# Optimization experiments

Hardware: AMD Instinct MI355X
Metric: run time of the kernel (lower is better)

The kernel has to match this reference:

```python
import jax, jax.numpy as jnp
import numpy as np

N_NODES = 100000
N_EDGES = 1600000
IN_FEATS = 128
N_HIDDEN = 128
N_CLASSES = 16


def setup_inputs() -> dict:
    key = jax.random.key(0)
    ks = jax.random.split(key, 10)
    features = jax.random.normal(ks[0], (N_NODES, IN_FEATS), dtype=jnp.float32)
    src = jax.random.randint(ks[1], (N_EDGES,), 0, N_NODES, dtype=jnp.int32)
    dst = jax.random.randint(ks[2], (N_EDGES,), 0, N_NODES, dtype=jnp.int32)
    # Glorot-ish init for the three GraphConv layers
    def glorot(k, fan_in, fan_out):
        s = (2.0 / (fan_in + fan_out)) ** 0.5
        return jax.random.normal(k, (fan_in, fan_out), dtype=jnp.float32) * s
    W0 = glorot(ks[3], IN_FEATS, N_HIDDEN)
    b0 = jnp.zeros((N_HIDDEN,), jnp.float32)
    W1 = glorot(ks[4], N_HIDDEN, N_HIDDEN)
    b1 = jnp.zeros((N_HIDDEN,), jnp.float32)
    W2 = glorot(ks[5], N_HIDDEN, N_CLASSES)
    b2 = jnp.zeros((N_CLASSES,), jnp.float32)
    return {"features": features, "src": src, "dst": dst,
            "W0": W0, "b0": b0, "W1": W1, "b1": b1, "W2": W2, "b2": b2}


def _graph_conv(h, src, dst, src_norm, dst_norm, W, b, act):
    # DGL GraphConv, norm='both':
    # out = D_dst^{-1/2} * sum_{(u->v) in E} (D_src^{-1/2} h)_u W  + b
    h = h * src_norm[:, None]           # [N, F] scale by out-degree^-1/2
    hw = h @ W                          # [N, F_out] transform before gather (F_out <= F here)
    agg = jax.ops.segment_sum(hw[src], dst, num_segments=h.shape[0])  # scatter-add over edges
    out = agg * dst_norm[:, None] + b
    return act(out)


def reference(features, src, dst, W0, b0, W1, b1, W2, b2):
    N = features.shape[0]
    ones = jnp.ones(src.shape[0], dtype=jnp.float32)
    out_deg = jnp.clip(jax.ops.segment_sum(ones, src, num_segments=N), 1.0)
    in_deg = jnp.clip(jax.ops.segment_sum(ones, dst, num_segments=N), 1.0)
    src_norm = out_deg ** -0.5
    dst_norm = in_deg ** -0.5

    relu = jax.nn.relu
    pos_sigmoid = lambda x: jax.nn.sigmoid(x) + 1e-8

    h = features.astype(jnp.float32)
    h = _graph_conv(h, src, dst, src_norm, dst_norm, W0, b0, relu)
    h = _graph_conv(h, src, dst, src_norm, dst_norm, W1, b1, relu)
    h = _graph_conv(h, src, dst, src_norm, dst_norm, W2, b2, pos_sigmoid)
    return h
```

## Files before the change

### kernel.cpp

```cpp
#include <hip/hip_runtime.h>
#include <hip/hip_bf16.h>


constexpr int BLK = 256;
constexpr int CH = 8192;

typedef __attribute__((ext_vector_type(8))) short s8v;
typedef __attribute__((ext_vector_type(4))) float f4v;

__device__ __forceinline__ float bflo(unsigned int u) { return __uint_as_float(u << 16); }
__device__ __forceinline__ float bfhi(unsigned int u) { return __uint_as_float(u & 0xffff0000u); }
__device__ __forceinline__ unsigned int bfr(float f) {
    unsigned int u = __float_as_uint(f);
    return (u + 0x7fffu + ((u >> 16) & 1u)) >> 16;
}
__device__ __forceinline__ unsigned int bfpack(float lo, float hi) {
    unsigned int ul = __float_as_uint(lo), uh = __float_as_uint(hi);
    unsigned int rl = (ul + 0x7fffu + ((ul >> 16) & 1u)) >> 16;
    unsigned int rh = (uh + 0x7fffu + ((uh >> 16) & 1u)) & 0xffff0000u;
    return rl | rh;
}

__global__ __launch_bounds__(256) void k_pcount(const int* __restrict__ src, const int* __restrict__ dst,
                                                int* __restrict__ pmat_d, int* __restrict__ pmat_s,
                                                int E, int NB) {
    __shared__ int hd[1024], hs[1024];
    for (int i = threadIdx.x; i < 1024; i += 256) { hd[i] = 0; hs[i] = 0; }
    __syncthreads();
    int b = blockIdx.x;
    int e0 = b * CH, e1 = min(e0 + CH, E);
    for (int e = e0 + threadIdx.x; e < e1; e += 256) {
        atomicAdd(&hd[dst[e] >> 7], 1);
        atomicAdd(&hs[src[e] >> 7], 1);
    }
    __syncthreads();
    for (int i = threadIdx.x; i < NB; i += 256) {
        pmat_d[(size_t)b * NB + i] = hd[i];
        pmat_s[(size_t)b * NB + i] = hs[i];
    }
}

__global__ __launch_bounds__(1024) void k_pscan1(const int* __restrict__ pmat_d, const int* __restrict__ pmat_s,
                                                 int* __restrict__ bbase_d, int* __restrict__ bbase_s,
                                                 int NB, int nblk) {
    const int* pmat = blockIdx.x ? pmat_s : pmat_d;
    int* bbase = blockIdx.x ? bbase_s : bbase_d;
    __shared__ int s[1024];
    int t = threadIdx.x;
    int tot = 0;
    if (t < NB) {
#pragma unroll 8
        for (int b = 0; b < nblk; b++) tot += pmat[(size_t)b * NB + t];
    }
    s[t] = (t < NB) ? tot : 0;
    __syncthreads();
    for (int d = 1; d < 1024; d <<= 1) {
        int x = (t >= d) ? s[t - d] : 0;
        __syncthreads();
        s[t] += x;
        __syncthreads();
    }
    if (t < NB) {
        bbase[t] = s[t] - tot;
        if (t == NB - 1) bbase[NB] = s[t];
    }
}

__global__ __launch_bounds__(256) void k_pscan2(const int* __restrict__ pmat_d, const int* __restrict__ pmat_s,
                                                const int* __restrict__ bbase_d, const int* __restrict__ bbase_s,
                                                int* __restrict__ omat_d, int* __restrict__ omat_s,
                                                int NB, int nblk) {
    int which = blockIdx.x & 1;
    int t = (blockIdx.x >> 1) * 256 + threadIdx.x;
    const int* pmat = which ? pmat_s : pmat_d;
    const int* bbase = which ? bbase_s : bbase_d;
    int* omat = which ? omat_s : omat_d;
    if (t >= NB) return;
    int run = bbase[t];
#pragma unroll 8
    for (int b = 0; b < nblk; b++) {
        size_t idx = (size_t)b * NB + t;
        omat[idx] = run;
        run += pmat[idx];
    }
}

__global__ __launch_bounds__(256) void k_pscatter(const int* __restrict__ src, const int* __restrict__ dst,
                                                  const int* __restrict__ omat_d, const int* __restrict__ omat_s,
                                                  unsigned int* __restrict__ ebuf_d, unsigned char* __restrict__ ebuf_s,
                                                  int E, int NB) {
    __shared__ int cd[1024], cs[1024];
    int b = blockIdx.x;
    for (int i = threadIdx.x; i < NB; i += 256) {
        cd[i] = omat_d[(size_t)b * NB + i];
        cs[i] = omat_s[(size_t)b * NB + i];
    }
    __syncthreads();
    int e0 = b * CH, e1 = min(e0 + CH, E);
    for (int e = e0 + threadIdx.x; e < e1; e += 256) {
        int s_ = src[e], d_ = dst[e];
        int pd = atomicAdd(&cd[d_ >> 7], 1);
        ebuf_d[pd] = (unsigned)s_ | ((unsigned)(d_ & 127) << 17);
        int ps = atomicAdd(&cs[s_ >> 7], 1);
        ebuf_s[ps] = (unsigned char)(s_ & 127);
    }
}

__global__ __launch_bounds__(256) void k_bcount(const unsigned char* __restrict__ ebuf_s,
                                                const int* __restrict__ bbase_s,
                                                float* __restrict__ srcn, int N) {
    __shared__ int cnt[128];
    int k = blockIdx.x;
    if (threadIdx.x < 128) cnt[threadIdx.x] = 0;
    __syncthreads();
    int beg = bbase_s[k], end = bbase_s[k + 1];
    for (int i = beg + threadIdx.x; i < end; i += 256) atomicAdd(&cnt[ebuf_s[i]], 1);
    __syncthreads();
    if (threadIdx.x < 128) {
        int v = k * 128 + threadIdx.x;
        if (v < N) {
            int c = cnt[threadIdx.x];
            if (c < 1) c = 1;
            srcn[v] = rsqrtf((float)c);
        }
    }
}

__global__ __launch_bounds__(256) void k_sortcsr(const unsigned int* __restrict__ ebuf,
                                                 const int* __restrict__ bbase,
                                                 int* __restrict__ csr, int* __restrict__ rowptr,
                                                 int N, int E) {
    __shared__ unsigned int rec[4096];
    __shared__ unsigned int sorted[4096];
    __shared__ int cnt[128];
    __shared__ int wstart[129];
    __shared__ int wcur[128];
    int k = blockIdx.x, tx = threadIdx.x;
    int ebeg = bbase[k];
    int ecnt = bbase[k + 1] - ebeg;
    if (ecnt > 4096) ecnt = 4096;
    if (tx < 128) cnt[tx] = 0;
    __syncthreads();
    for (int i = tx; i < ecnt; i += 256) {
        unsigned int r = ebuf[ebeg + i];
        rec[i] = r;
        atomicAdd(&cnt[(r >> 17) & 127], 1);
    }
    __syncthreads();
    if (tx < 128) wcur[tx] = cnt[tx];
    __syncthreads();
    for (int d = 1; d < 128; d <<= 1) {
        int x = (tx < 128 && tx >= d) ? wcur[tx - d] : 0;
        __syncthreads();
        if (tx < 128) wcur[tx] += x;
        __syncthreads();
    }
    if (tx < 128) wstart[tx] = wcur[tx] - cnt[tx];
    if (tx == 127) wstart[128] = wcur[127];
    __syncthreads();
    if (tx < 128) wcur[tx] = wstart[tx];
    __syncthreads();
    for (int i = tx; i < ecnt; i += 256) {
        unsigned int r = rec[i];
        int p = atomicAdd(&wcur[(r >> 17) & 127], 1);
        sorted[p] = r & 0x1FFFFu;
    }
    __syncthreads();
    for (int i = tx; i < ecnt; i += 256) csr[ebeg + i] = (int)sorted[i];
    if (tx < 128) {
        int v = k * 128 + tx;
        if (v < N) rowptr[v] = ebeg + wstart[tx];
    }
    if (k == (int)gridDim.x - 1 && tx == 0) rowptr[N] = E;
}

__global__ void k_wt3(const float* __restrict__ W0, const float* __restrict__ W1, const float* __restrict__ W2,
                      unsigned short* __restrict__ Wt0, unsigned short* __restrict__ Wt1,
                      unsigned short* __restrict__ Wt2) {
    int b = blockIdx.x;
    const float* W; unsigned short* Wt; int total, base;
    if (b < 64)      { W = W0; Wt = Wt0; total = 16384; base = b * 256; }
    else if (b < 128){ W = W1; Wt = Wt1; total = 16384; base = (b - 64) * 256; }
    else             { W = W2; Wt = Wt2; total = 2048;  base = (b - 128) * 256; }
    int i = base + threadIdx.x;
    if (i < total) {
        int Ncol = total >> 7;
        int c = i >> 7, k = i & 127;
        Wt[i] = (unsigned short)bfr(W[k * Ncol + c]);
    }
}

template <int NT, int F32IN>
__global__ __launch_bounds__(256) void k_gemm_mfma(const unsigned short* __restrict__ Ab,
                                                   const float* __restrict__ Af,
                                                   const float* __restrict__ srcn,
                                                   const unsigned short* __restrict__ Wt,
                                                   unsigned short* __restrict__ outb, int M) {
    __shared__ unsigned short As[64 * 128];
    __shared__ unsigned short Ws[NT * 16 * 128];
    int tx = threadIdx.x;
    int row0 = blockIdx.x * 64;
    for (int p = 0; p < NT; ++p) {
        int r = p * 16 + (tx >> 4);
        int c = tx & 15;
        int cs = c ^ (r & 7);
        *(uint4*)(&Ws[(r * 16 + cs) * 8]) = *(const uint4*)(Wt + (size_t)r * 128 + c * 8);
    }
    for (int p = 0; p < 4; ++p) {
        int r = p * 16 + (tx >> 4);
        int c = tx & 15;
        int cs = c ^ (r & 7);
        int gr = row0 + r;
        uint4 v = make_uint4(0u, 0u, 0u, 0u);
        if (gr < M) {
            if (F32IN) {
                const float4* pf = (const float4*)(Af + (size_t)gr * 128 + c * 8);
                float4 a = pf[0], b = pf[1];
                float s = srcn[gr];
                v.x = bfpack(a.x * s, a.y * s);
                v.y = bfpack(a.z * s, a.w * s);
                v.z = bfpack(b.x * s, b.y * s);
                v.w = bfpack(b.z * s, b.w * s);
            } else {
                v = *(const uint4*)(Ab + (size_t)gr * 128 + c * 8);
            }
        }
        *(uint4*)(&As[(r * 16 + cs) * 8]) = v;
    }
    __syncthreads();

    int w = tx >> 6, l = tx & 63;
    int lr = l & 15, lg = l >> 4;
    f4v acc[NT];
#pragma unroll
    for (int nt = 0; nt < NT; ++nt) { acc[nt][0] = 0.f; acc[nt][1] = 0.f; acc[nt][2] = 0.f; acc[nt][3] = 0.f; }

    int ar = w * 16 + lr;
#pragma unroll
    for (int kk = 0; kk < 4; ++kk) {
        s8v af = *(const s8v*)(&As[(ar * 16 + ((kk * 4 + lg) ^ (ar & 7))) * 8]);
#pragma unroll
        for (int nt = 0; nt < NT; ++nt) {
            int br = nt * 16 + lr;
            s8v bf = *(const s8v*)(&Ws[(br * 16 + ((kk * 4 + lg) ^ (br & 7))) * 8]);
            acc[nt] = __builtin_amdgcn_mfma_f32_16x16x32_bf16(af, bf, acc[nt], 0, 0, 0);
        }
    }
#pragma unroll
    for (int nt = 0; nt < NT; ++nt) {
#pragma unroll
        for (int i = 0; i < 4; ++i) {
            int R = row0 + w * 16 + lg * 4 + i;
            if (R < M) {
                int col = nt * 16 + lr;
                outb[(size_t)R * (NT * 16) + col] = (unsigned short)bfr(acc[nt][i]);
            }
        }
    }
}

__global__ __launch_bounds__(256) void k_aggN(const unsigned short* __restrict__ hw,
                                              const int* __restrict__ csr,
                                              const int* __restrict__ rowptr,
                                              const float* __restrict__ srcn,
                                              const float* __restrict__ bias,
                                              unsigned short* __restrict__ out, int N) {
    int t = blockIdx.x * 256 + threadIdx.x;
    int v = t >> 4, sub = t & 15;
    if (v >= N) return;
    int s0 = rowptr[v], s1 = rowptr[v + 1];

    float a0 = 0.f, a1 = 0.f, a2 = 0.f, a3 = 0.f, a4 = 0.f, a5 = 0.f, a6 = 0.f, a7 = 0.f;
#define ACC8(V)                                                         \
    a0 += bflo(V.x); a1 += bfhi(V.x); a2 += bflo(V.y); a3 += bfhi(V.y); \
    a4 += bflo(V.z); a5 += bfhi(V.z); a6 += bflo(V.w); a7 += bfhi(V.w);
    int e = s0;
    for (; e + 4 <= s1; e += 4) {
        int x0 = csr[e], x1 = csr[e + 1], x2 = csr[e + 2], x3 = csr[e + 3];
        uint4 v0 = *(const uint4*)(hw + (size_t)x0 * 128 + sub * 8);
        uint4 v1 = *(const uint4*)(hw + (size_t)x1 * 128 + sub * 8);
        uint4 v2 = *(const uint4*)(hw + (size_t)x2 * 128 + sub * 8);
        uint4 v3 = *(const uint4*)(hw + (size_t)x3 * 128 + sub * 8);
        ACC8(v0) ACC8(v1) ACC8(v2) ACC8(v3)
    }
    for (; e < s1; ++e) {
        int x0 = csr[e];
        uint4 v0 = *(const uint4*)(hw + (size_t)x0 * 128 + sub * 8);
        ACC8(v0)
    }
#undef ACC8
    int deg = s1 - s0;
    if (deg < 1) deg = 1;
    float dn = rsqrtf((float)deg);
    float4 b0 = *(const float4*)(bias + sub * 8);
    float4 b1 = *(const float4*)(bias + sub * 8 + 4);
    float sn = srcn[v];
    float o0 = fmaxf(a0 * dn + b0.x, 0.f) * sn, o1 = fmaxf(a1 * dn + b0.y, 0.f) * sn;
    float o2 = fmaxf(a2 * dn + b0.z, 0.f) * sn, o3 = fmaxf(a3 * dn + b0.w, 0.f) * sn;
    float o4 = fmaxf(a4 * dn + b1.x, 0.f) * sn, o5 = fmaxf(a5 * dn + b1.y, 0.f) * sn;
    float o6 = fmaxf(a6 * dn + b1.z, 0.f) * sn, o7 = fmaxf(a7 * dn + b1.w, 0.f) * sn;
    uint4 o;
    o.x = bfpack(o0, o1); o.y = bfpack(o2, o3);
    o.z = bfpack(o4, o5); o.w = bfpack(o6, o7);
    *(uint4*)(out + (size_t)v * 128 + sub * 8) = o;
}

__global__ __launch_bounds__(256) void k_agg16(const unsigned short* __restrict__ hw,
                                               const int* __restrict__ csr,
                                               const int* __restrict__ rowptr,
                                               const float* __restrict__ bias,
                                               float* __restrict__ out, int N) {
    int t = blockIdx.x * 256 + threadIdx.x;
    int v = t >> 2, q = t & 3;
    if (v >= N) return;
    int s0 = rowptr[v], s1 = rowptr[v + 1];
    float a0 = 0.f, a1 = 0.f, a2 = 0.f, a3 = 0.f;
#define ACC4(V)                                                         \
    a0 += bflo(V.x); a1 += bfhi(V.x); a2 += bflo(V.y); a3 += bfhi(V.y);
    int e = s0;
    for (; e + 4 <= s1; e += 4) {
        int x0 = csr[e], x1 = csr[e + 1], x2 = csr[e + 2], x3 = csr[e + 3];
        uint2 v0 = *(const uint2*)(hw + (size_t)x0 * 16 + q * 4);
        uint2 v1 = *(const uint2*)(hw + (size_t)x1 * 16 + q * 4);
        uint2 v2 = *(const uint2*)(hw + (size_t)x2 * 16 + q * 4);
        uint2 v3 = *(const uint2*)(hw + (size_t)x3 * 16 + q * 4);
        ACC4(v0) ACC4(v1) ACC4(v2) ACC4(v3)
    }
    for (; e < s1; ++e) {
        int x0 = csr[e];
        uint2 v0 = *(const uint2*)(hw + (size_t)x0 * 16 + q * 4);
        ACC4(v0)
    }
#undef ACC4
    int deg = s1 - s0;
    if (deg < 1) deg = 1;
    float dn = rsqrtf((float)deg);
    float4 b = *(const float4*)(bias + q * 4);
    float o0 = 1.f / (1.f + __expf(-(a0 * dn + b.x))) + 1e-8f;
    float o1 = 1.f / (1.f + __expf(-(a1 * dn + b.y))) + 1e-8f;
    float o2 = 1.f / (1.f + __expf(-(a2 * dn + b.z))) + 1e-8f;
    float o3 = 1.f / (1.f + __expf(-(a3 * dn + b.w))) + 1e-8f;
    *(float4*)(out + (size_t)v * 16 + q * 4) = make_float4(o0, o1, o2, o3);
}

extern "C" void kernel_launch(void* const* d_in, const int* in_sizes, int n_in,
                              void* d_out, int out_size, void* d_ws, size_t ws_size,
                              hipStream_t stream) {
    const float* features = (const float*)d_in[0];
    const int*   src      = (const int*)d_in[1];
    const int*   dst      = (const int*)d_in[2];
    const float* W0       = (const float*)d_in[3];
    const float* b0       = (const float*)d_in[4];
    const float* W1       = (const float*)d_in[5];
    const float* b1       = (const float*)d_in[6];
    const float* W2       = (const float*)d_in[7];
    const float* b2       = (const float*)d_in[8];
    float* out = (float*)d_out;

    const int N = in_sizes[0] / 128;
    const int E = in_sizes[1];
    const int NB = (N + 127) >> 7;
    const int nblk = (E + CH - 1) / CH;

    char* ws = (char*)d_ws;
    size_t off = 0;
    auto alloc = [&](size_t bytes) -> char* {
        char* p = ws + off;
        off += (bytes + 255) / 256 * 256;
        return p;
    };
    int* pmat_d  = (int*)alloc((size_t)nblk * NB * 4);
    int* pmat_s  = (int*)alloc((size_t)nblk * NB * 4);
    int* omat_d  = (int*)alloc((size_t)nblk * NB * 4);
    int* omat_s  = (int*)alloc((size_t)nblk * NB * 4);
    int* bbase_d = (int*)alloc((size_t)(NB + 1) * 4);
    int* bbase_s = (int*)alloc((size_t)(NB + 1) * 4);
    unsigned int*  ebuf_d = (unsigned int*)alloc((size_t)E * 4);
    unsigned char* ebuf_s = (unsigned char*)alloc((size_t)E);
    int* csr     = (int*)alloc((size_t)E * 4);
    int* rowptr  = (int*)alloc((size_t)(N + 1) * 4);
    float* srcn  = (float*)alloc((size_t)N * 4);
    unsigned short* Wt0 = (unsigned short*)alloc(128 * 128 * 2);
    unsigned short* Wt1 = (unsigned short*)alloc(128 * 128 * 2);
    unsigned short* Wt2 = (unsigned short*)alloc(16 * 128 * 2);
    unsigned short* B1 = (unsigned short*)alloc((size_t)N * 128 * 2);
    unsigned short* B2 = (unsigned short*)alloc((size_t)N * 128 * 2);
    unsigned short* HW16 = (unsigned short*)alloc((size_t)N * 16 * 2);
    (void)ws_size; (void)n_in; (void)out_size;

    k_pcount<<<nblk, 256, 0, stream>>>(src, dst, pmat_d, pmat_s, E, NB);
    k_pscan1<<<2, 1024, 0, stream>>>(pmat_d, pmat_s, bbase_d, bbase_s, NB, nblk);
    k_pscan2<<<2 * ((NB + 255) / 256), 256, 0, stream>>>(pmat_d, pmat_s, bbase_d, bbase_s, omat_d, omat_s, NB, nblk);
    k_pscatter<<<nblk, 256, 0, stream>>>(src, dst, omat_d, omat_s, ebuf_d, ebuf_s, E, NB);
    k_bcount<<<NB, 256, 0, stream>>>(ebuf_s, bbase_s, srcn, N);
    k_sortcsr<<<NB, 256, 0, stream>>>(ebuf_d, bbase_d, csr, rowptr, N, E);
    k_wt3<<<136, 256, 0, stream>>>(W0, W1, W2, Wt0, Wt1, Wt2);

    int gb = (N + 63) / 64;
    int anb = (N * 16 + 255) / 256;
    int a16b = (N * 4 + 255) / 256;

    k_gemm_mfma<8, 1><<<gb, 256, 0, stream>>>(nullptr, features, srcn, Wt0, B2, N);
    k_aggN<<<anb, 256, 0, stream>>>(B2, csr, rowptr, srcn, b0, B1, N);
    k_gemm_mfma<8, 0><<<gb, 256, 0, stream>>>(B1, nullptr, nullptr, Wt1, B2, N);
    k_aggN<<<anb, 256, 0, stream>>>(B2, csr, rowptr, srcn, b1, B1, N);
    k_gemm_mfma<1, 0><<<gb, 256, 0, stream>>>(B1, nullptr, nullptr, Wt2, HW16, N);
    k_agg16<<<a16b, 256, 0, stream>>>(HW16, csr, rowptr, b2, out, N);
}
```

Baseline: 351.7 us.

## Fuse preprocessing kernels, pad CSR rows to 4, and loop GEMM over strips

Merges the two scan kernels into one and fuses CSR sort, source-degree counting and weight transpose into a single multi-role launch, which removes several launches. CSR rows are padded to a multiple of four with a dummy zeroed node row at index N. The aggregation kernels can then load four neighbour indices as one int4 and drop the scalar tail loop. The GEMM kernel now processes four 64-row strips per block, so the weight tile staged in shared memory is reused across strips. The costs are extra padded gathers of the zero row and a cap of 3584 edges per 128-node bucket, which could truncate rows on skewed graphs.

```diff
diff --git a/kernel.cpp b/kernel.cpp
--- a/kernel.cpp
+++ b/kernel.cpp
@@ -40,11 +40,14 @@
     }
 }
 
-__global__ __launch_bounds__(1024) void k_pscan1(const int* __restrict__ pmat_d, const int* __restrict__ pmat_s,
-                                                 int* __restrict__ bbase_d, int* __restrict__ bbase_s,
-                                                 int NB, int nblk) {
+__global__ __launch_bounds__(1024) void k_pscan(const int* __restrict__ pmat_d, const int* __restrict__ pmat_s,
+                                                int* __restrict__ bbase_d, int* __restrict__ bbase_s,
+                                                int* __restrict__ omat_d, int* __restrict__ omat_s,
+                                                unsigned short* __restrict__ B2pad, unsigned short* __restrict__ HW16pad,
+                                                int N, int NB, int nblk) {
     const int* pmat = blockIdx.x ? pmat_s : pmat_d;
     int* bbase = blockIdx.x ? bbase_s : bbase_d;
+    int* omat  = blockIdx.x ? omat_s : omat_d;
     __shared__ int s[1024];
     int t = threadIdx.x;
     int tot = 0;
@@ -61,27 +64,20 @@
         __syncthreads();
     }
     if (t < NB) {
-        bbase[t] = s[t] - tot;
+        int base = s[t] - tot;
+        bbase[t] = base;
         if (t == NB - 1) bbase[NB] = s[t];
-    }
-}
-
-__global__ __launch_bounds__(256) void k_pscan2(const int* __restrict__ pmat_d, const int* __restrict__ pmat_s,
-                                                const int* __restrict__ bbase_d, const int* __restrict__ bbase_s,
-                                                int* __restrict__ omat_d, int* __restrict__ omat_s,
-                                                int NB, int nblk) {
-    int which = blockIdx.x & 1;
-    int t = (blockIdx.x >> 1) * 256 + threadIdx.x;
-    const int* pmat = which ? pmat_s : pmat_d;
-    const int* bbase = which ? bbase_s : bbase_d;
-    int* omat = which ? omat_s : omat_d;
-    if (t >= NB) return;
-    int run = bbase[t];
+        int run = base;
 #pragma unroll 8
-    for (int b = 0; b < nblk; b++) {
-        size_t idx = (size_t)b * NB + t;
-        omat[idx] = run;
-        run += pmat[idx];
+        for (int b = 0; b < nblk; b++) {
+            size_t idx = (size_t)b * NB + t;
+            omat[idx] = run;
+            run += pmat[idx];
+        }
+    }
+    if (blockIdx.x == 1) {
+        if (t < 128) B2pad[(size_t)N * 128 + t] = 0;
+        if (t < 16)  HW16pad[(size_t)N * 16 + t] = 0;
     }
 }
 
@@ -106,87 +102,92 @@
     }
 }
 
-__global__ __launch_bounds__(256) void k_bcount(const unsigned char* __restrict__ ebuf_s,
-                                                const int* __restrict__ bbase_s,
-                                                float* __restrict__ srcn, int N) {
-    __shared__ int cnt[128];
-    int k = blockIdx.x;
-    if (threadIdx.x < 128) cnt[threadIdx.x] = 0;
-    __syncthreads();
-    int beg = bbase_s[k], end = bbase_s[k + 1];
-    for (int i = beg + threadIdx.x; i < end; i += 256) atomicAdd(&cnt[ebuf_s[i]], 1);
-    __syncthreads();
-    if (threadIdx.x < 128) {
-        int v = k * 128 + threadIdx.x;
-        if (v < N) {
-            int c = cnt[threadIdx.x];
-            if (c < 1) c = 1;
-            srcn[v] = rsqrtf((float)c);
-        }
-    }
-}
-
-__global__ __launch_bounds__(256) void k_sortcsr(const unsigned int* __restrict__ ebuf,
-                                                 const int* __restrict__ bbase,
-                                                 int* __restrict__ csr, int* __restrict__ rowptr,
-                                                 int N, int E) {
-    __shared__ unsigned int rec[4096];
-    __shared__ unsigned int sorted[4096];
-    __shared__ int cnt[128];
-    __shared__ int wstart[129];
-    __shared__ int wcur[128];
-    int k = blockIdx.x, tx = threadIdx.x;
-    int ebeg = bbase[k];
-    int ecnt = bbase[k + 1] - ebeg;
-    if (ecnt > 4096) ecnt = 4096;
-    if (tx < 128) cnt[tx] = 0;
-    __syncthreads();
-    for (int i = tx; i < ecnt; i += 256) {
-        unsigned int r = ebuf[ebeg + i];
-        rec[i] = r;
-        atomicAdd(&cnt[(r >> 17) & 127], 1);
-    }
-    __syncthreads();
-    if (tx < 128) wcur[tx] = cnt[tx];
-    __syncthreads();
-    for (int d = 1; d < 128; d <<= 1) {
-        int x = (tx < 128 && tx >= d) ? wcur[tx - d] : 0;
-        __syncthreads();
-        if (tx < 128) wcur[tx] += x;
-        __syncthreads();
-    }
-    if (tx < 128) wstart[tx] = wcur[tx] - cnt[tx];
-    if (tx == 127) wstart[128] = wcur[127];
-    __syncthreads();
-    if (tx < 128) wcur[tx] = wstart[tx];
-    __syncthreads();
-    for (int i = tx; i < ecnt; i += 256) {
-        unsigned int r = rec[i];
-        int p = atomicAdd(&wcur[(r >> 17) & 127], 1);
-        sorted[p] = r & 0x1FFFFu;
-    }
-    __syncthreads();
-    for (int i = tx; i < ecnt; i += 256) csr[ebeg + i] = (int)sorted[i];
-    if (tx < 128) {
-        int v = k * 128 + tx;
-        if (v < N) rowptr[v] = ebeg + wstart[tx];
-    }
-    if (k == (int)gridDim.x - 1 && tx == 0) rowptr[N] = E;
-}
-
-__global__ void k_wt3(const float* __restrict__ W0, const float* __restrict__ W1, const float* __restrict__ W2,
-                      unsigned short* __restrict__ Wt0, unsigned short* __restrict__ Wt1,
-                      unsigned short* __restrict__ Wt2) {
-    int b = blockIdx.x;
-    const float* W; unsigned short* Wt; int total, base;
-    if (b < 64)      { W = W0; Wt = Wt0; total = 16384; base = b * 256; }
-    else if (b < 128){ W = W1; Wt = Wt1; total = 16384; base = (b - 64) * 256; }
-    else             { W = W2; Wt = Wt2; total = 2048;  base = (b - 128) * 256; }
-    int i = base + threadIdx.x;
-    if (i < total) {
-        int Ncol = total >> 7;
-        int c = i >> 7, k = i & 127;
-        Wt[i] = (unsigned short)bfr(W[k * Ncol + c]);
+__global__ __launch_bounds__(256) void k_build(const unsigned int* __restrict__ ebuf_d,
+                                               const int* __restrict__ bbase_d,
+                                               const unsigned char* __restrict__ ebuf_s,
+                                               const int* __restrict__ bbase_s,
+                                               int* __restrict__ csr, int* __restrict__ rowptr,
+                                               int* __restrict__ deg, float* __restrict__ srcn,
+                                               const float* __restrict__ W0, const float* __restrict__ W1,
+                                               const float* __restrict__ W2,
+                                               unsigned short* __restrict__ Wt0, unsigned short* __restrict__ Wt1,
+                                               unsigned short* __restrict__ Wt2,
+                                               int N, int NB) {
+    int b = blockIdx.x, tx = threadIdx.x;
+    if (b < NB) {
+        __shared__ unsigned int rec[3584];
+        __shared__ unsigned int sorted[4096];
+        __shared__ int cnt[128];
+        __shared__ int pws[129];
+        __shared__ int wcur[128];
+        int k = b;
+        int ebeg = bbase_d[k];
+        int ecnt = bbase_d[k + 1] - ebeg;
+        if (ecnt > 3584) ecnt = 3584;
+        int pbase = ((ebeg + 3) & ~3) + k * 512;
+        if (tx < 128) cnt[tx] = 0;
+        __syncthreads();
+        for (int i = tx; i < ecnt; i += 256) {
+            unsigned int r = ebuf_d[ebeg + i];
+            rec[i] = r;
+            atomicAdd(&cnt[(r >> 17) & 127], 1);
+        }
+        __syncthreads();
+        int pc = (tx < 128) ? ((cnt[tx] + 3) & ~3) : 0;
+        if (tx < 128) wcur[tx] = pc;
+        __syncthreads();
+        for (int d = 1; d < 128; d <<= 1) {
+            int x = (tx < 128 && tx >= d) ? wcur[tx - d] : 0;
+            __syncthreads();
+            if (tx < 128) wcur[tx] += x;
+            __syncthreads();
+        }
+        if (tx < 128) pws[tx] = wcur[tx] - pc;
+        if (tx == 127) pws[128] = wcur[127];
+        __syncthreads();
+        int pecnt = pws[128];
+        for (int i = tx; i < pecnt; i += 256) sorted[i] = (unsigned)N;
+        if (tx < 128) wcur[tx] = pws[tx];
+        __syncthreads();
+        for (int i = tx; i < ecnt; i += 256) {
+            unsigned int r = rec[i];
+            int p = atomicAdd(&wcur[(r >> 17) & 127], 1);
+            sorted[p] = r & 0x1FFFFu;
+        }
+        __syncthreads();
+        for (int i = tx; i < pecnt; i += 256) csr[pbase + i] = (int)sorted[i];
+        if (tx < 128) {
+            int v = k * 128 + tx;
+            if (v < N) { rowptr[v] = pbase + pws[tx]; deg[v] = cnt[tx]; }
+        }
+    } else if (b < 2 * NB) {
+        __shared__ int scnt[128];
+        int k = b - NB;
+        if (tx < 128) scnt[tx] = 0;
+        __syncthreads();
+        int beg = bbase_s[k], end = bbase_s[k + 1];
+        for (int i = beg + tx; i < end; i += 256) atomicAdd(&scnt[ebuf_s[i]], 1);
+        __syncthreads();
+        if (tx < 128) {
+            int v = k * 128 + tx;
+            if (v < N) {
+                int c = scnt[tx];
+                if (c < 1) c = 1;
+                srcn[v] = rsqrtf((float)c);
+            }
+        }
+    } else {
+        int bb = b - 2 * NB;
+        const float* W; unsigned short* Wt; int total, base;
+        if (bb < 64)      { W = W0; Wt = Wt0; total = 16384; base = bb * 256; }
+        else if (bb < 128){ W = W1; Wt = Wt1; total = 16384; base = (bb - 64) * 256; }
+        else              { W = W2; Wt = Wt2; total = 2048;  base = (bb - 128) * 256; }
+        int i = base + tx;
+        if (i < total) {
+            int Ncol = total >> 7;
+            int c = i >> 7, kk = i & 127;
+            Wt[i] = (unsigned short)bfr(W[kk * Ncol + c]);
+        }
     }
 }
 
@@ -196,64 +197,67 @@
                                                    const float* __restrict__ srcn,
                                                    const unsigned short* __restrict__ Wt,
                                                    unsigned short* __restrict__ outb, int M) {
+    __shared__ unsigned short Ws[NT * 16 * 128];
     __shared__ unsigned short As[64 * 128];
-    __shared__ unsigned short Ws[NT * 16 * 128];
     int tx = threadIdx.x;
-    int row0 = blockIdx.x * 64;
     for (int p = 0; p < NT; ++p) {
         int r = p * 16 + (tx >> 4);
         int c = tx & 15;
         int cs = c ^ (r & 7);
         *(uint4*)(&Ws[(r * 16 + cs) * 8]) = *(const uint4*)(Wt + (size_t)r * 128 + c * 8);
     }
-    for (int p = 0; p < 4; ++p) {
-        int r = p * 16 + (tx >> 4);
-        int c = tx & 15;
-        int cs = c ^ (r & 7);
-        int gr = row0 + r;
-        uint4 v = make_uint4(0u, 0u, 0u, 0u);
-        if (gr < M) {
-            if (F32IN) {
-                const float4* pf = (const float4*)(Af + (size_t)gr * 128 + c * 8);
-                float4 a = pf[0], b = pf[1];
-                float s = srcn[gr];
-                v.x = bfpack(a.x * s, a.y * s);
-                v.y = bfpack(a.z * s, a.w * s);
-                v.z = bfpack(b.x * s, b.y * s);
-                v.w = bfpack(b.z * s, b.w * s);
-            } else {
-                v = *(const uint4*)(Ab + (size_t)gr * 128 + c * 8);
-            }
-        }
-        *(uint4*)(&As[(r * 16 + cs) * 8]) = v;
-    }
-    __syncthreads();
-
     int w = tx >> 6, l = tx & 63;
     int lr = l & 15, lg = l >> 4;
-    f4v acc[NT];
+    int ar = w * 16 + lr;
+
+    for (int strip = 0; strip < 4; ++strip) {
+        int row0 = blockIdx.x * 256 + strip * 64;
+        __syncthreads();
+        for (int p = 0; p < 4; ++p) {
+            int r = p * 16 + (tx >> 4);
+            int c = tx & 15;
+            int cs = c ^ (r & 7);
+            int gr = row0 + r;
+            uint4 v = make_uint4(0u, 0u, 0u, 0u);
+            if (gr < M) {
+                if (F32IN) {
+                    const float4* pf = (const float4*)(Af + (size_t)gr * 128 + c * 8);
+                    float4 a = pf[0], bq = pf[1];
+                    float s = srcn[gr];
+                    v.x = bfpack(a.x * s, a.y * s);
+                    v.y = bfpack(a.z * s, a.w * s);
+                    v.z = bfpack(bq.x * s, bq.y * s);
+                    v.w = bfpack(bq.z * s, bq.w * s);
+                } else {
+                    v = *(const uint4*)(Ab + (size_t)gr * 128 + c * 8);
+                }
+            }
+            *(uint4*)(&As[(r * 16 + cs) * 8]) = v;
+        }
+        __syncthreads();
+
+        f4v acc[NT];
 #pragma unroll
-    for (int nt = 0; nt < NT; ++nt) { acc[nt][0] = 0.f; acc[nt][1] = 0.f; acc[nt][2] = 0.f; acc[nt][3] = 0.f; }
-
-    int ar = w * 16 + lr;
+        for (int nt = 0; nt < NT; ++nt) { acc[nt][0] = 0.f; acc[nt][1] = 0.f; acc[nt][2] = 0.f; acc[nt][3] = 0.f; }
 #pragma unroll
-    for (int kk = 0; kk < 4; ++kk) {
-        s8v af = *(const s8v*)(&As[(ar * 16 + ((kk * 4 + lg) ^ (ar & 7))) * 8]);
+        for (int kk = 0; kk < 4; ++kk) {
+            s8v af = *(const s8v*)(&As[(ar * 16 + ((kk * 4 + lg) ^ (ar & 7))) * 8]);
+#pragma unroll
+            for (int nt = 0; nt < NT; ++nt) {
+                int br = nt * 16 + lr;
+                s8v bf = *(const s8v*)(&Ws[(br * 16 + ((kk * 4 + lg) ^ (br & 7))) * 8]);
+                acc[nt] = __builtin_amdgcn_mfma_f32_16x16x32_bf16(af, bf, acc[nt], 0, 0, 0);
+            }
+        }
 #pragma unroll
         for (int nt = 0; nt < NT; ++nt) {
-            int br = nt * 16 + lr;
-            s8v bf = *(const s8v*)(&Ws[(br * 16 + ((kk * 4 + lg) ^ (br & 7))) * 8]);
-            acc[nt] = __builtin_amdgcn_mfma_f32_16x16x32_bf16(af, bf, acc[nt], 0, 0, 0);
-        }
-    }
 #pragma unroll
-    for (int nt = 0; nt < NT; ++nt) {
-#pragma unroll
-        for (int i = 0; i < 4; ++i) {
-            int R = row0 + w * 16 + lg * 4 + i;
-            if (R < M) {
-                int col = nt * 16 + lr;
-                outb[(size_t)R * (NT * 16) + col] = (unsigned short)bfr(acc[nt][i]);
+            for (int i = 0; i < 4; ++i) {
+                int R = row0 + w * 16 + lg * 4 + i;
+                if (R < M) {
+                    int col = nt * 16 + lr;
+                    outb[(size_t)R * (NT * 16) + col] = (unsigned short)bfr(acc[nt][i]);
+                }
             }
         }
     }
@@ -262,36 +266,33 @@
 __global__ __launch_bounds__(256) void k_aggN(const unsigned short* __restrict__ hw,
                                               const int* __restrict__ csr,
                                               const int* __restrict__ rowptr,
+                                              const int* __restrict__ deg,
                                               const float* __restrict__ srcn,
                                               const float* __restrict__ bias,
                                               unsigned short* __restrict__ out, int N) {
     int t = blockIdx.x * 256 + threadIdx.x;
     int v = t >> 4, sub = t & 15;
     if (v >= N) return;
-    int s0 = rowptr[v], s1 = rowptr[v + 1];
+    int s0 = rowptr[v];
+    int dg = deg[v];
+    int plen = (dg + 3) & ~3;
+    const unsigned short* hws = hw + sub * 8;
 
     float a0 = 0.f, a1 = 0.f, a2 = 0.f, a3 = 0.f, a4 = 0.f, a5 = 0.f, a6 = 0.f, a7 = 0.f;
 #define ACC8(V)                                                         \
     a0 += bflo(V.x); a1 += bfhi(V.x); a2 += bflo(V.y); a3 += bfhi(V.y); \
     a4 += bflo(V.z); a5 += bfhi(V.z); a6 += bflo(V.w); a7 += bfhi(V.w);
-    int e = s0;
-    for (; e + 4 <= s1; e += 4) {
-        int x0 = csr[e], x1 = csr[e + 1], x2 = csr[e + 2], x3 = csr[e + 3];
-        uint4 v0 = *(const uint4*)(hw + (size_t)x0 * 128 + sub * 8);
-        uint4 v1 = *(const uint4*)(hw + (size_t)x1 * 128 + sub * 8);
-        uint4 v2 = *(const uint4*)(hw + (size_t)x2 * 128 + sub * 8);
-        uint4 v3 = *(const uint4*)(hw + (size_t)x3 * 128 + sub * 8);
+    for (int e = s0; e < s0 + plen; e += 4) {
+        int4 xs = *(const int4*)(csr + e);
+        uint4 v0 = *(const uint4*)(hws + (size_t)xs.x * 128);
+        uint4 v1 = *(const uint4*)(hws + (size_t)xs.y * 128);
+        uint4 v2 = *(const uint4*)(hws + (size_t)xs.z * 128);
+        uint4 v3 = *(const uint4*)(hws + (size_t)xs.w * 128);
         ACC8(v0) ACC8(v1) ACC8(v2) ACC8(v3)
     }
-    for (; e < s1; ++e) {
-        int x0 = csr[e];
-        uint4 v0 = *(const uint4*)(hw + (size_t)x0 * 128 + sub * 8);
-        ACC8(v0)
-    }
 #undef ACC8
-    int deg = s1 - s0;
-    if (deg < 1) deg = 1;
-    float dn = rsqrtf((float)deg);
+    int d = dg < 1 ? 1 : dg;
+    float dn = rsqrtf((float)d);
     float4 b0 = *(const float4*)(bias + sub * 8);
     float4 b1 = *(const float4*)(bias + sub * 8 + 4);
     float sn = srcn[v];
@@ -308,33 +309,30 @@
 __global__ __launch_bounds__(256) void k_agg16(const unsigned short* __restrict__ hw,
                                                const int* __restrict__ csr,
                                                const int* __restrict__ rowptr,
+                                               const int* __restrict__ deg,
                                                const float* __restrict__ bias,
                                                float* __restrict__ out, int N) {
     int t = blockIdx.x * 256 + threadIdx.x;
     int v = t >> 2, q = t & 3;
     if (v >= N) return;
-    int s0 = rowptr[v], s1 = rowptr[v + 1];
+    int s0 = rowptr[v];
+    int dg = deg[v];
+    int plen = (dg + 3) & ~3;
+    const unsigned short* hws = hw + q * 4;
     float a0 = 0.f, a1 = 0.f, a2 = 0.f, a3 = 0.f;
 #define ACC4(V)                                                         \
     a0 += bflo(V.x); a1 += bfhi(V.x); a2 += bflo(V.y); a3 += bfhi(V.y);
-    int e = s0;
-    for (; e + 4 <= s1; e += 4) {
-        int x0 = csr[e], x1 = csr[e + 1], x2 = csr[e + 2], x3 = csr[e + 3];
-        uint2 v0 = *(const uint2*)(hw + (size_t)x0 * 16 + q * 4);
-        uint2 v1 = *(const uint2*)(hw + (size_t)x1 * 16 + q * 4);
-        uint2 v2 = *(const uint2*)(hw + (size_t)x2 * 16 + q * 4);
-        uint2 v3 = *(const uint2*)(hw + (size_t)x3 * 16 + q * 4);
+    for (int e = s0; e < s0 + plen; e += 4) {
+        int4 xs = *(const int4*)(csr + e);
+        uint2 v0 = *(const uint2*)(hws + (size_t)xs.x * 16);
+        uint2 v1 = *(const uint2*)(hws + (size_t)xs.y * 16);
+        uint2 v2 = *(const uint2*)(hws + (size_t)xs.z * 16);
+        uint2 v3 = *(const uint2*)(hws + (size_t)xs.w * 16);
         ACC4(v0) ACC4(v1) ACC4(v2) ACC4(v3)
     }
-    for (; e < s1; ++e) {
-        int x0 = csr[e];
-        uint2 v0 = *(const uint2*)(hw + (size_t)x0 * 16 + q * 4);
-        ACC4(v0)
-    }
 #undef ACC4
-    int deg = s1 - s0;
-    if (deg < 1) deg = 1;
-    float dn = rsqrtf((float)deg);
+    int d = dg < 1 ? 1 : dg;
+    float dn = rsqrtf((float)d);
     float4 b = *(const float4*)(bias + q * 4);
     float o0 = 1.f / (1.f + __expf(-(a0 * dn + b.x))) + 1e-8f;
     float o1 = 1.f / (1.f + __expf(-(a1 * dn + b.y))) + 1e-8f;
@@ -377,33 +375,32 @@
     int* bbase_s = (int*)alloc((size_t)(NB + 1) * 4);
     unsigned int*  ebuf_d = (unsigned int*)alloc((size_t)E * 4);
     unsigned char* ebuf_s = (unsigned char*)alloc((size_t)E);
-    int* csr     = (int*)alloc((size_t)E * 4);
+    int* csr     = (int*)alloc(((size_t)E + (size_t)NB * 512 + 512) * 4);
     int* rowptr  = (int*)alloc((size_t)(N + 1) * 4);
+    int* deg     = (int*)alloc((size_t)N * 4);
     float* srcn  = (float*)alloc((size_t)N * 4);
     unsigned short* Wt0 = (unsigned short*)alloc(128 * 128 * 2);
     unsigned short* Wt1 = (unsigned short*)alloc(128 * 128 * 2);
     unsigned short* Wt2 = (unsigned short*)alloc(16 * 128 * 2);
     unsigned short* B1 = (unsigned short*)alloc((size_t)N * 128 * 2);
-    unsigned short* B2 = (unsigned short*)alloc((size_t)N * 128 * 2);
-    unsigned short* HW16 = (unsigned short*)alloc((size_t)N * 16 * 2);
+    unsigned short* B2 = (unsigned short*)alloc((size_t)(N + 1) * 128 * 2);
+    unsigned short* HW16 = (unsigned short*)alloc((size_t)(N + 1) * 16 * 2);
     (void)ws_size; (void)n_in; (void)out_size;
 
     k_pcount<<<nblk, 256, 0, stream>>>(src, dst, pmat_d, pmat_s, E, NB);
-    k_pscan1<<<2, 1024, 0, stream>>>(pmat_d, pmat_s, bbase_d, bbase_s, NB, nblk);
-    k_pscan2<<<2 * ((NB + 255) / 256), 256, 0, stream>>>(pmat_d, pmat_s, bbase_d, bbase_s, omat_d, omat_s, NB, nblk);
+    k_pscan<<<2, 1024, 0, stream>>>(pmat_d, pmat_s, bbase_d, bbase_s, omat_d, omat_s, B2, HW16, N, NB, nblk);
     k_pscatter<<<nblk, 256, 0, stream>>>(src, dst, omat_d, omat_s, ebuf_d, ebuf_s, E, NB);
-    k_bcount<<<NB, 256, 0, stream>>>(ebuf_s, bbase_s, srcn, N);
-    k_sortcsr<<<NB, 256, 0, stream>>>(ebuf_d, bbase_d, csr, rowptr, N, E);
-    k_wt3<<<136, 256, 0, stream>>>(W0, W1, W2, Wt0, Wt1, Wt2);
-
-    int gb = (N + 63) / 64;
+    k_build<<<2 * NB + 136, 256, 0, stream>>>(ebuf_d, bbase_d, ebuf_s, bbase_s, csr, rowptr, deg, srcn,
+                                              W0, W1, W2, Wt0, Wt1, Wt2, N, NB);
+
+    int gb = (N + 255) / 256;
     int anb = (N * 16 + 255) / 256;
     int a16b = (N * 4 + 255) / 256;
 
     k_gemm_mfma<8, 1><<<gb, 256, 0, stream>>>(nullptr, features, srcn, Wt0, B2, N);
-    k_aggN<<<anb, 256, 0, stream>>>(B2, csr, rowptr, srcn, b0, B1, N);
+    k_aggN<<<anb, 256, 0, stream>>>(B2, csr, rowptr, deg, srcn, b0, B1, N);
     k_gemm_mfma<8, 0><<<gb, 256, 0, stream>>>(B1, nullptr, nullptr, Wt1, B2, N);
-    k_aggN<<<anb, 256, 0, stream>>>(B2, csr, rowptr, srcn, b1, B1, N);
+    k_aggN<<<anb, 256, 0, stream>>>(B2, csr, rowptr, deg, srcn, b1, B1, N);
     k_gemm_mfma<1, 0><<<gb, 256, 0, stream>>>(B1, nullptr, nullptr, Wt2, HW16, N);
-    k_agg16<<<a16b, 256, 0, stream>>>(HW16, csr, rowptr, b2, out, N);
-}
+    k_agg16<<<a16b, 256, 0, stream>>>(HW16, csr, rowptr, deg, b2, out, N);
+}
```

New measurement: 357.8 us. About the same (+1.7%).
